# Performance work log

Measured on AMD Instinct MI355X. Metric: run time of the kernel, lower is better.

The kernel has to match this reference:

```python
import jax, jax.numpy as jnp
import numpy as np

K = 3                      # kernel size
PAD = 1
GAIN = 1.4142135623730951  # torch calculate_gain('relu') = sqrt(2)
STD_SPATIAL = GAIN / K     # FilterNorm spatial, running_std=False -> scalar
EPS = 1e-10
NEG_SLOPE = 0.1
RES_SCALE = 1.0


def _filter_norm_spatial(f):
    # f: [B, K*K, H, W]; normalize across the K*K filter channels per pixel
    m = f.mean(axis=1, keepdims=True)
    s = f.std(axis=1, keepdims=True, ddof=1)  # torch std is unbiased
    return (f - m) / (s + EPS) * STD_SPATIAL


def _filter_norm_channel(f, std_ch, C):
    # f: [B, C*K*K]; normalize over the K*K taps of each channel
    B = f.shape[0]
    f = f.reshape(B, C, K * K)
    m = f.mean(axis=2, keepdims=True)
    s = f.std(axis=2, keepdims=True, ddof=1)
    f = (f - m) / (s + EPS)
    return f.reshape(B, -1) * std_ch  # learned per-element std (running_std=True)


def _ddf_mul(x, cf, sf):
    # x: [B,C,H,W], cf: [B,C,K*K], sf: [B,K*K,H,W]
    # out[b,c,i,j] = sum_t x_pad[b,c,i+u(t),j+v(t)] * cf[b,c,t] * sf[b,t,i,j]
    B, C, H, W = x.shape
    xp = jnp.pad(x, ((0, 0), (0, 0), (PAD, PAD), (PAD, PAD)))
    out = jnp.zeros_like(x)
    for t in range(K * K):  # small fixed loop over 9 taps
        u, v = t // K, t % K
        patch = xp[:, :, u:u + H, v:v + W]
        out = out + patch * cf[:, :, t, None, None] * sf[:, t:t + 1, :, :]
    return out


def _ddfpack(x, Ws, bs, W1, b1, W2, b2, std_ch):
    B, C, H, W = x.shape
    # spatial branch: 1x1 conv C -> K*K, then FilterNorm('spatial')
    sf = jnp.einsum('bchw,kc->bkhw', x, Ws) + bs[None, :, None, None]
    sf = _filter_norm_spatial(sf)
    # channel branch: GAP -> fc -> relu -> fc -> FilterNorm('channel')
    pooled = x.mean(axis=(2, 3))                       # [B, C]
    h = jax.nn.relu(pooled @ W1.T + b1)                # [B, mid]
    cf = h @ W2.T + b2                                 # [B, C*K*K]
    cf = _filter_norm_channel(cf, std_ch, C).reshape(B, C, K * K)
    return _ddf_mul(x, cf, sf)


def setup_inputs() -> dict:
    key = jax.random.key(0)
    ks = jax.random.split(key, 10)
    B, C, H, W = 16, 64, 192, 192
    mid = int(C * 0.2)  # se_ratio = 0.2 -> 12
    return {
        'x': jax.random.normal(ks[0], (B, C, H, W), jnp.float32),
        'Ws': jax.random.normal(ks[1], (K * K, C), jnp.float32) * 0.1,
        'bs': jax.random.normal(ks[2], (K * K,), jnp.float32) * 0.1,
        'W1': jax.random.normal(ks[3], (mid, C), jnp.float32) * 0.1,
        'b1': jax.random.normal(ks[4], (mid,), jnp.float32) * 0.1,
        'W2': jax.random.normal(ks[5], (C * K * K, mid), jnp.float32) * 0.1,
        'b2': jax.random.normal(ks[6], (C * K * K,), jnp.float32) * 0.1,
        'std_ch': jax.random.normal(ks[7], (C * K * K,), jnp.float32) * STD_SPATIAL,
        'Wc': jax.random.normal(ks[8], (C, C, K, K), jnp.float32) * 0.05,
        'bc': jax.random.normal(ks[9], (C,), jnp.float32) * 0.05,
    }


def reference(x, Ws, bs, W1, b1, W2, b2, std_ch, Wc, bc):
    out = _ddfpack(x, Ws, bs, W1, b1, W2, b2, std_ch)
    out = jnp.where(out >= 0, out, NEG_SLOPE * out)  # LeakyReLU(0.1)
    out = jax.lax.conv_general_dilated(
        out, Wc, window_strides=(1, 1), padding='SAME',
        dimension_numbers=('NCHW', 'OIHW', 'NCHW'))
    out = out + bc[None, :, None, None]
    return x + out * RES_SCALE
```

## Files before the change

kernel.cpp:

```cpp
#include <hip/hip_runtime.h>

typedef unsigned short ushort_t;
typedef unsigned int uint_t;

typedef __attribute__((ext_vector_type(8))) __bf16 bf16x8;
typedef __attribute__((ext_vector_type(4))) float f32x4;

#define HH 192
#define WW 192
#define HWD (192*192)
#define CC 64
#define BB 16

__device__ __forceinline__ float b2f(uint_t u) {
    return __uint_as_float((u & 0xffffu) << 16);
}
__device__ __forceinline__ ushort_t f2b(float f) {
    uint_t x = __float_as_uint(f);
    uint_t r = x + 0x7fffu + ((x >> 16) & 1u);
    return (ushort_t)(r >> 16);
}
__device__ __forceinline__ bf16x8 zero8() {
    uint4 z; z.x = 0; z.y = 0; z.z = 0; z.w = 0;
    return __builtin_bit_cast(bf16x8, z);
}
__device__ __forceinline__ bf16x8 ld8(const ushort_t* p) {
    return __builtin_bit_cast(bf16x8, *(const uint4*)p);
}

__global__ void k_prep(const float* __restrict__ Wc, ushort_t* __restrict__ wt) {
    int i = blockIdx.x * 256 + threadIdx.x;
    if (i < 9 * 64 * 64) {
        int t  = i >> 12;
        int co = (i >> 6) & 63;
        int ci = i & 63;
        wt[i] = f2b(Wc[(co * 64 + ci) * 9 + t]);
    }
}

__global__ void k_pool(const float* __restrict__ x, float* __restrict__ pooled) {
    int c = blockIdx.x, b = blockIdx.y, tid = threadIdx.x;
    const float4* xp = (const float4*)(x + (size_t)(b * 64 + c) * HWD);
    float s = 0.f;
    for (int i = tid; i < HWD / 4; i += 256) {
        float4 u = xp[i];
        s += u.x + u.y + u.z + u.w;
    }
    __shared__ float red[4];
    for (int o = 32; o > 0; o >>= 1) s += __shfl_down(s, o, 64);
    if ((tid & 63) == 0) red[tid >> 6] = s;
    __syncthreads();
    if (tid == 0) pooled[b * 64 + c] = (red[0] + red[1] + red[2] + red[3]) * (1.f / (float)HWD);
}

__global__ void k_mlp(const float* __restrict__ pooled,
                      const float* __restrict__ W1, const float* __restrict__ b1,
                      const float* __restrict__ W2, const float* __restrict__ b2,
                      const float* __restrict__ std_ch, float* __restrict__ cf) {
    int b = blockIdx.x, tid = threadIdx.x;
    __shared__ float pl[64], hv[12];
    pl[tid] = pooled[b * 64 + tid];
    __syncthreads();
    if (tid < 12) {
        float h = b1[tid];
        for (int c = 0; c < 64; c++) h += pl[c] * W1[tid * 64 + c];
        hv[tid] = h > 0.f ? h : 0.f;
    }
    __syncthreads();
    int c = tid;
    float r[9]; float m = 0.f;
    #pragma unroll
    for (int t = 0; t < 9; t++) {
        float v = b2[c * 9 + t];
        #pragma unroll
        for (int k = 0; k < 12; k++) v += hv[k] * W2[(c * 9 + t) * 12 + k];
        r[t] = v; m += v;
    }
    m *= (1.f / 9.f);
    float var = 0.f;
    #pragma unroll
    for (int t = 0; t < 9; t++) { float d = r[t] - m; var += d * d; }
    var *= (1.f / 8.f);
    float inv = 1.f / (sqrtf(var) + 1e-10f);
    #pragma unroll
    for (int t = 0; t < 9; t++)
        cf[(b * 64 + c) * 9 + t] = (r[t] - m) * inv * std_ch[c * 9 + t];
}

__global__ __launch_bounds__(256, 2)
void k_fused(const float* __restrict__ x, const float* __restrict__ Ws,
             const float* __restrict__ bs, const float* __restrict__ cf,
             ushort_t* __restrict__ y) {
    __shared__ ushort_t xt[64 * 434];
    __shared__ float sfL[256 * 12];
    __shared__ float WsL[576];
    __shared__ float cfL[576];
    __shared__ float bsL[9];

    int b = blockIdx.y;
    int tw = blockIdx.x % 3, th = blockIdx.x / 3;
    int h0 = th * 4, w0 = tw * 64;
    int tid = threadIdx.x;

    for (int i = tid; i < 576; i += 256) { WsL[i] = Ws[i]; cfL[i] = cf[b * 576 + i]; }
    if (tid < 9) bsL[tid] = bs[tid];

    const float* xb = x + (size_t)b * 64 * HWD;
    #pragma unroll
    for (int j = 0; j < 27; j++) {
        int idx = tid + j * 256;
        int c = idx / 108;
        int rem = idx - c * 108;
        int r = rem / 18, seg = rem - r * 18;
        int gr = h0 - 1 + r;
        int gw0 = w0 - 4 + seg * 4;
        float4 v;
        if (gr >= 0 && gr < HH && gw0 >= 0 && gw0 < WW)
            v = *(const float4*)(xb + (size_t)c * HWD + (size_t)gr * WW + gw0);
        else { v.x = 0.f; v.y = 0.f; v.z = 0.f; v.w = 0.f; }
        int o = c * 434 + r * 72 + seg * 4;
        *(uint_t*)(&xt[o])     = (uint_t)f2b(v.x) | ((uint_t)f2b(v.y) << 16);
        *(uint_t*)(&xt[o + 2]) = (uint_t)f2b(v.z) | ((uint_t)f2b(v.w) << 16);
    }
    __syncthreads();

    {
        int hl = tid >> 6, wl = tid & 63;
        float s[9];
        #pragma unroll
        for (int t = 0; t < 9; t++) s[t] = bsL[t];
        int base = (hl + 1) * 72 + wl + 4;
        for (int c = 0; c < 64; c++) {
            float xv = b2f(xt[c * 434 + base]);
            #pragma unroll
            for (int t = 0; t < 9; t++) s[t] += xv * WsL[t * 64 + c];
        }
        float m = 0.f;
        #pragma unroll
        for (int t = 0; t < 9; t++) m += s[t];
        m *= (1.f / 9.f);
        float var = 0.f;
        #pragma unroll
        for (int t = 0; t < 9; t++) { float d = s[t] - m; var += d * d; }
        var *= (1.f / 8.f);
        float inv = 0.4714045207910317f / (sqrtf(var) + 1e-10f);
        #pragma unroll
        for (int t = 0; t < 9; t++) sfL[tid * 12 + t] = (s[t] - m) * inv;
    }
    __syncthreads();

    int lane = tid & 63;
    int hl = tid >> 6;
    float cfv[9];
    #pragma unroll
    for (int t = 0; t < 9; t++) cfv[t] = cfL[lane * 9 + t];
    const uint_t* lds32 = (const uint_t*)xt;
    int gh = h0 + hl;
    size_t yrow = ((size_t)b * HWD + (size_t)gh * WW + w0) * 64 + lane;

    for (int k = 0; k < 64; k++) {
        const f32x4* sp = (const f32x4*)&sfL[(hl * 64 + k) * 12];
        f32x4 s0 = sp[0], s1 = sp[1];
        float s8 = sfL[(hl * 64 + k) * 12 + 8];
        float wv[9];
        wv[0] = cfv[0] * s0[0]; wv[1] = cfv[1] * s0[1]; wv[2] = cfv[2] * s0[2];
        wv[3] = cfv[3] * s0[3]; wv[4] = cfv[4] * s1[0]; wv[5] = cfv[5] * s1[1];
        wv[6] = cfv[6] * s1[2]; wv[7] = cfv[7] * s1[3]; wv[8] = cfv[8] * s8;

        int p0 = k + 3;
        int a = p0 & ~1;
        bool odd = (p0 & 1) != 0;
        float acc = 0.f;
        #pragma unroll
        for (int r = 0; r < 3; r++) {
            int di = lane * 217 + (hl + r) * 36 + (a >> 1);
            uint_t d0 = lds32[di], d1 = lds32[di + 1];
            float v0 = b2f(d0), v1 = b2f(d0 >> 16), v2 = b2f(d1), v3 = b2f(d1 >> 16);
            float xa = odd ? v1 : v0;
            float xm = odd ? v2 : v1;
            float xc = odd ? v3 : v2;
            acc += xa * wv[r * 3 + 0] + xm * wv[r * 3 + 1] + xc * wv[r * 3 + 2];
        }
        float v = acc >= 0.f ? acc : 0.1f * acc;
        y[yrow + (size_t)k * 64] = f2b(v);
    }
}

#define CONV_LDS_BYTES (6 * 66 * 128)

__global__ __launch_bounds__(256, 2)
void k_conv(const ushort_t* __restrict__ y, const ushort_t* __restrict__ wt,
            const float* __restrict__ x, const float* __restrict__ bc,
            float* __restrict__ out) {
    __shared__ char yt[CONV_LDS_BYTES];

    int bid = blockIdx.x;
    int swz = (bid & 7) * 288 + (bid >> 3);
    int b = swz / 144;
    int rem = swz - b * 144;
    int ht = rem / 3;
    int wtile = rem - ht * 3;
    int h0 = ht * 4, w0 = wtile * 64;

    int tid = threadIdx.x;
    int lane = tid & 63, ln = lane & 15, quad = lane >> 4;
    int wv_ = tid >> 6, phi = wv_ & 1, rr = wv_ >> 1;

    const ushort_t* yb = y + (size_t)b * HWD * 64;
    #pragma unroll
    for (int j = 0; j < 13; j++) {
        int i = tid + j * 256;
        if (i < 6 * 66 * 8) {
            int row = i / 528;
            int r2 = i - row * 528;
            int p = r2 >> 3, c = r2 & 7;
            int gh = h0 - 1 + row, gw = w0 - 1 + p;
            uint4 v;
            if (gh >= 0 && gh < HH && gw >= 0 && gw < WW)
                v = *(const uint4*)(yb + ((size_t)(gh * WW + gw) * 64 + c * 8));
            else { v.x = 0; v.y = 0; v.z = 0; v.w = 0; }
            int off = ((row * 66 + p) << 7) + ((c ^ (p & 7)) << 4);
            *(uint4*)(yt + off) = v;
        }
    }

    bf16x8 wf[9][2][2];
    #pragma unroll
    for (int t = 0; t < 9; t++)
        #pragma unroll
        for (int ks = 0; ks < 2; ks++)
            #pragma unroll
            for (int mt = 0; mt < 2; mt++) {
                int co = phi * 32 + mt * 16 + ln;
                wf[t][ks][mt] = ld8(wt + ((t * 64 + co) * 64 + ks * 32 + quad * 8));
            }
    float bcv[2][4];
    #pragma unroll
    for (int mt = 0; mt < 2; mt++)
        #pragma unroll
        for (int r = 0; r < 4; r++)
            bcv[mt][r] = bc[phi * 32 + mt * 16 + quad * 4 + r];

    __syncthreads();

    for (int orr = 0; orr < 2; orr++) {
        int orow = rr * 2 + orr;
        int gh = h0 + orow;
        #pragma unroll
        for (int s = 0; s < 4; s++) {
            size_t o0 = (size_t)(b * 64 + phi * 32) * HWD + (size_t)gh * WW + w0 + s * 16 + ln;
            float xv[2][4];
            #pragma unroll
            for (int mt = 0; mt < 2; mt++)
                #pragma unroll
                for (int r = 0; r < 4; r++)
                    xv[mt][r] = x[o0 + (size_t)(mt * 16 + quad * 4 + r) * HWD];

            f32x4 acc[2];
            #pragma unroll
            for (int mt = 0; mt < 2; mt++) {
                acc[mt][0] = bcv[mt][0]; acc[mt][1] = bcv[mt][1];
                acc[mt][2] = bcv[mt][2]; acc[mt][3] = bcv[mt][3];
            }

            #pragma unroll
            for (int t = 0; t < 9; t++) {
                const int u_ = t / 3, v_ = t % 3;
                int p = s * 16 + ln + v_;
                int boff = ((orow + u_) * 66 + p) << 7;
                int a0 = boff + ((quad ^ (p & 7)) << 4);
                int a1 = a0 ^ 64;
                bf16x8 f0 = __builtin_bit_cast(bf16x8, *(const uint4*)(yt + a0));
                bf16x8 f1 = __builtin_bit_cast(bf16x8, *(const uint4*)(yt + a1));
                acc[0] = __builtin_amdgcn_mfma_f32_16x16x32_bf16(wf[t][0][0], f0, acc[0], 0, 0, 0);
                acc[1] = __builtin_amdgcn_mfma_f32_16x16x32_bf16(wf[t][0][1], f0, acc[1], 0, 0, 0);
                acc[0] = __builtin_amdgcn_mfma_f32_16x16x32_bf16(wf[t][1][0], f1, acc[0], 0, 0, 0);
                acc[1] = __builtin_amdgcn_mfma_f32_16x16x32_bf16(wf[t][1][1], f1, acc[1], 0, 0, 0);
            }

            #pragma unroll
            for (int mt = 0; mt < 2; mt++)
                #pragma unroll
                for (int r = 0; r < 4; r++)
                    out[o0 + (size_t)(mt * 16 + quad * 4 + r) * HWD] = acc[mt][r] + xv[mt][r];
        }
    }
}

extern "C" void kernel_launch(void* const* d_in, const int* in_sizes, int n_in,
                              void* d_out, int out_size, void* d_ws, size_t ws_size,
                              hipStream_t stream) {
    const float* x      = (const float*)d_in[0];
    const float* Ws     = (const float*)d_in[1];
    const float* bs     = (const float*)d_in[2];
    const float* W1     = (const float*)d_in[3];
    const float* b1     = (const float*)d_in[4];
    const float* W2     = (const float*)d_in[5];
    const float* b2     = (const float*)d_in[6];
    const float* std_ch = (const float*)d_in[7];
    const float* Wc     = (const float*)d_in[8];
    const float* bc     = (const float*)d_in[9];
    float* out = (float*)d_out;

    char* ws = (char*)d_ws;
    float*    pooled = (float*)(ws);
    float*    cf     = (float*)(ws + 4096);
    ushort_t* wt     = (ushort_t*)(ws + 40960);
    ushort_t* y      = (ushort_t*)(ws + 131072);

    k_prep<<<dim3(144), dim3(256), 0, stream>>>(Wc, wt);
    k_pool<<<dim3(64, 16), dim3(256), 0, stream>>>(x, pooled);
    k_mlp<<<dim3(16), dim3(64), 0, stream>>>(pooled, W1, b1, W2, b2, std_ch, cf);
    k_fused<<<dim3(144, 16), dim3(256), 0, stream>>>(x, Ws, bs, cf, y);
    k_conv<<<dim3(2304), dim3(256), 0, stream>>>(y, wt, x, bc, out);
}
```

Measured before the change: 513.3 us.

## Restructure conv loop to stream weights per tap and raise occupancy

Swaps the conv loop order. Instead of holding all 9 taps of weight fragments in registers (36 bf16x8), each tap's four weight fragments are loaded inside a non-unrolled tap loop, and 16 accumulators for all row/segment tiles are kept live. This lowers register pressure so the launch bound can rise from 2 to 3 blocks per SM for better latency hiding. In exchange, weights are reloaded from global/L2 for every tap per block, the 9-tap loop is no longer unrolled, and the accumulators hold more registers.

After: 495.7 us. 1.04x faster.

```diff
diff --git a/kernel.cpp b/kernel.cpp
--- a/kernel.cpp
+++ b/kernel.cpp
@@ -188,7 +188,7 @@
 
 #define CONV_LDS_BYTES (6 * 66 * 128)
 
-__global__ __launch_bounds__(256, 2)
+__global__ __launch_bounds__(256, 3)
 void k_conv(const ushort_t* __restrict__ y, const ushort_t* __restrict__ wt,
             const float* __restrict__ x, const float* __restrict__ bc,
             float* __restrict__ out) {
@@ -204,7 +204,7 @@
 
     int tid = threadIdx.x;
     int lane = tid & 63, ln = lane & 15, quad = lane >> 4;
-    int wv_ = tid >> 6, phi = wv_ & 1, rr = wv_ >> 1;
+    int wv_ = tid >> 6, phi = wv_ & 1, rp = wv_ >> 1;
 
     const ushort_t* yb = y + (size_t)b * HWD * 64;
     #pragma unroll
@@ -224,65 +224,67 @@
         }
     }
 
-    bf16x8 wf[9][2][2];
-    #pragma unroll
-    for (int t = 0; t < 9; t++)
-        #pragma unroll
-        for (int ks = 0; ks < 2; ks++)
+    float bcv[2][4];
+    #pragma unroll
+    for (int mt = 0; mt < 2; mt++)
+        #pragma unroll
+        for (int r = 0; r < 4; r++)
+            bcv[mt][r] = bc[phi * 32 + mt * 16 + quad * 4 + r];
+
+    __syncthreads();
+
+    f32x4 acc[2][4][2];
+    #pragma unroll
+    for (int row = 0; row < 2; row++)
+        #pragma unroll
+        for (int s = 0; s < 4; s++)
             #pragma unroll
             for (int mt = 0; mt < 2; mt++) {
-                int co = phi * 32 + mt * 16 + ln;
-                wf[t][ks][mt] = ld8(wt + ((t * 64 + co) * 64 + ks * 32 + quad * 8));
+                acc[row][s][mt][0] = bcv[mt][0]; acc[row][s][mt][1] = bcv[mt][1];
+                acc[row][s][mt][2] = bcv[mt][2]; acc[row][s][mt][3] = bcv[mt][3];
             }
-    float bcv[2][4];
-    #pragma unroll
-    for (int mt = 0; mt < 2; mt++)
-        #pragma unroll
-        for (int r = 0; r < 4; r++)
-            bcv[mt][r] = bc[phi * 32 + mt * 16 + quad * 4 + r];
-
-    __syncthreads();
-
-    for (int orr = 0; orr < 2; orr++) {
-        int orow = rr * 2 + orr;
-        int gh = h0 + orow;
+
+    #pragma unroll 1
+    for (int t = 0; t < 9; t++) {
+        bf16x8 wf00 = ld8(wt + ((t * 64 + phi * 32 + ln) * 64      + quad * 8));
+        bf16x8 wf01 = ld8(wt + ((t * 64 + phi * 32 + ln) * 64 + 32 + quad * 8));
+        bf16x8 wf10 = ld8(wt + ((t * 64 + phi * 32 + 16 + ln) * 64      + quad * 8));
+        bf16x8 wf11 = ld8(wt + ((t * 64 + phi * 32 + 16 + ln) * 64 + 32 + quad * 8));
+        int u_ = t / 3, v_ = t % 3;
+        #pragma unroll
+        for (int row = 0; row < 2; row++) {
+            int ra = rp * 2 + row + u_;
+            #pragma unroll
+            for (int s = 0; s < 4; s++) {
+                int p = s * 16 + ln + v_;
+                int a0 = ((ra * 66 + p) << 7) + ((quad ^ (p & 7)) << 4);
+                bf16x8 f0 = __builtin_bit_cast(bf16x8, *(const uint4*)(yt + a0));
+                bf16x8 f1 = __builtin_bit_cast(bf16x8, *(const uint4*)(yt + (a0 ^ 64)));
+                acc[row][s][0] = __builtin_amdgcn_mfma_f32_16x16x32_bf16(wf00, f0, acc[row][s][0], 0, 0, 0);
+                acc[row][s][1] = __builtin_amdgcn_mfma_f32_16x16x32_bf16(wf10, f0, acc[row][s][1], 0, 0, 0);
+                acc[row][s][0] = __builtin_amdgcn_mfma_f32_16x16x32_bf16(wf01, f1, acc[row][s][0], 0, 0, 0);
+                acc[row][s][1] = __builtin_amdgcn_mfma_f32_16x16x32_bf16(wf11, f1, acc[row][s][1], 0, 0, 0);
+            }
+        }
+    }
+
+    #pragma unroll
+    for (int row = 0; row < 2; row++) {
+        int gh = h0 + rp * 2 + row;
         #pragma unroll
         for (int s = 0; s < 4; s++) {
-            size_t o0 = (size_t)(b * 64 + phi * 32) * HWD + (size_t)gh * WW + w0 + s * 16 + ln;
-            float xv[2][4];
             #pragma unroll
-            for (int mt = 0; mt < 2; mt++)
+            for (int mt = 0; mt < 2; mt++) {
+                size_t o0 = (size_t)(b * 64 + phi * 32 + mt * 16) * HWD
+                          + (size_t)gh * WW + w0 + s * 16 + ln;
+                float xv[4];
                 #pragma unroll
                 for (int r = 0; r < 4; r++)
-                    xv[mt][r] = x[o0 + (size_t)(mt * 16 + quad * 4 + r) * HWD];
-
-            f32x4 acc[2];
-            #pragma unroll
-            for (int mt = 0; mt < 2; mt++) {
-                acc[mt][0] = bcv[mt][0]; acc[mt][1] = bcv[mt][1];
-                acc[mt][2] = bcv[mt][2]; acc[mt][3] = bcv[mt][3];
-            }
-
-            #pragma unroll
-            for (int t = 0; t < 9; t++) {
-                const int u_ = t / 3, v_ = t % 3;
-                int p = s * 16 + ln + v_;
-                int boff = ((orow + u_) * 66 + p) << 7;
-                int a0 = boff + ((quad ^ (p & 7)) << 4);
-                int a1 = a0 ^ 64;
-                bf16x8 f0 = __builtin_bit_cast(bf16x8, *(const uint4*)(yt + a0));
-                bf16x8 f1 = __builtin_bit_cast(bf16x8, *(const uint4*)(yt + a1));
-                acc[0] = __builtin_amdgcn_mfma_f32_16x16x32_bf16(wf[t][0][0], f0, acc[0], 0, 0, 0);
-                acc[1] = __builtin_amdgcn_mfma_f32_16x16x32_bf16(wf[t][0][1], f0, acc[1], 0, 0, 0);
-                acc[0] = __builtin_amdgcn_mfma_f32_16x16x32_bf16(wf[t][1][0], f1, acc[0], 0, 0, 0);
-                acc[1] = __builtin_amdgcn_mfma_f32_16x16x32_bf16(wf[t][1][1], f1, acc[1], 0, 0, 0);
-            }
-
-            #pragma unroll
-            for (int mt = 0; mt < 2; mt++)
+                    xv[r] = x[o0 + (size_t)(quad * 4 + r) * HWD];
                 #pragma unroll
                 for (int r = 0; r < 4; r++)
-                    out[o0 + (size_t)(mt * 16 + quad * 4 + r) * HWD] = acc[mt][r] + xv[mt][r];
+                    out[o0 + (size_t)(quad * 4 + r) * HWD] = acc[row][s][mt][r] + xv[r];
+            }
         }
     }
 }
```
